# Performance work log

Hardware: AMD Instinct MI355X
Metric: run time of the kernel (lower is better)

Reference implementation:

```python
import jax, jax.numpy as jnp
import numpy as np

N_NODES = 100000


def setup_inputs() -> dict:
    key = jax.random.key(0)
    k1, k2, k3, k4, k5, k6 = jax.random.split(key, 6)
    N, E, DIN, DOUT = N_NODES, 1600000, 64, 64
    feature = jax.random.normal(k1, (N, DIN), dtype=jnp.float32)
    norm = jax.random.uniform(k2, (N, 1), dtype=jnp.float32)  # per-node 1/sqrt(deg)-style norm
    src = jax.random.randint(k3, (E,), 0, N, dtype=jnp.int32)
    dst = jax.random.randint(k4, (E,), 0, N, dtype=jnp.int32)
    W = jax.random.normal(k5, (DOUT, DIN), dtype=jnp.float32) / jnp.sqrt(jnp.float32(DIN))
    b = jax.random.normal(k6, (DOUT,), dtype=jnp.float32)
    return {"feature": feature, "norm": norm, "src": src, "dst": dst, "W": W, "b": b}


def reference(feature, norm, src, dst, W, b):
    # message: h_src * norm_src, gathered per edge -> [E, DIN]
    msg = (feature * norm)[src]
    # reduce: scatter-sum over destination nodes, then renormalize by dst norm
    accum = jax.ops.segment_sum(msg, dst, num_segments=N_NODES) * norm  # [N, DIN]
    # final Linear: accum @ W^T + b
    return accum @ W.T + b
```

## Files before the change

kernel.cpp:

```cpp
#include <hip/hip_runtime.h>
#include <hip/hip_bf16.h>

#define N_NODES 100000
#define D 64
#define BNODES 128
#define NBKT 782
#define SCAP 16
#define SCAP2 32
#define FIXU 256
#define CAP 48
#define SENT 0xFFFFFFFFu

__global__ __launch_bounds__(1024) void pre_scatter_kernel(
    const float* __restrict__ feature,
    const float* __restrict__ norm,
    const float* __restrict__ W,
    const int* __restrict__ src, const int* __restrict__ dst,
    __hip_bfloat16* __restrict__ Zb,
    unsigned int* __restrict__ f1,
    unsigned int* __restrict__ f2,
    unsigned char* __restrict__ cnt,
    int E)
{
    __shared__ float Wt[D * 65];
    __shared__ unsigned int stage[NBKT][17];
    __shared__ int scnt[NBKT];

    const int bid = blockIdx.x;
    const int tid = threadIdx.x;

    for (int i = tid; i < NBKT; i += blockDim.x) scnt[i] = 0;
    for (int i = tid; i < D * D; i += blockDim.x) {
        int o = i >> 6, k = i & 63;
        Wt[k * 65 + o] = W[o * D + k];
    }
    __syncthreads();

    const int lane = tid & 63;
    const int wid  = tid >> 6;

    float wreg[D];
    #pragma unroll
    for (int k = 0; k < D; ++k) wreg[k] = Wt[k * 65 + lane];

    const int wave   = bid * 16 + wid;
    const int nwaves = FIXU * 16;
    for (int node = wave; node < N_NODES; node += nwaves) {
        const int nu = __builtin_amdgcn_readfirstlane(node);
        const float* __restrict__ fp = feature + (size_t)nu * D;
        float r = 0.f;
        #pragma unroll
        for (int j = 0; j < D / 4; ++j) {
            float4 a4 = *(const float4*)&fp[j * 4];
            r = fmaf(a4.x, wreg[4 * j + 0], r);
            r = fmaf(a4.y, wreg[4 * j + 1], r);
            r = fmaf(a4.z, wreg[4 * j + 2], r);
            r = fmaf(a4.w, wreg[4 * j + 3], r);
        }
        Zb[(size_t)nu * D + lane] = __float2bfloat16(r * norm[nu]);
    }

    const size_t ubase = (size_t)bid * NBKT;
    const int nthreads = FIXU * 1024;
    for (int e = bid * 1024 + tid; e < E; e += nthreads) {
        int t = dst[e];
        int b = t >> 7;
        unsigned u = ((unsigned)src[e] << 7) | (unsigned)(t & 127);
        int slot = atomicAdd(&scnt[b], 1);
        if (slot < SCAP) {
            stage[b][slot] = u;
        } else if (slot < SCAP2) {
            f2[(ubase + (size_t)b) * 16 + (slot - SCAP)] = u;
        }
    }
    __syncthreads();

    for (int idx = tid; idx < NBKT * 4; idx += blockDim.x) {
        int bb = idx >> 2, j = idx & 3;
        int n_live = scnt[bb];
        if (n_live > SCAP) n_live = SCAP;
        int base = j * 4;
        unsigned v0 = (base + 0 < n_live) ? stage[bb][base + 0] : SENT;
        unsigned v1 = (base + 1 < n_live) ? stage[bb][base + 1] : SENT;
        unsigned v2 = (base + 2 < n_live) ? stage[bb][base + 2] : SENT;
        unsigned v3 = (base + 3 < n_live) ? stage[bb][base + 3] : SENT;
        *(uint4*)&f1[(ubase + (size_t)bb) * 16 + base] =
            make_uint4(v0, v1, v2, v3);
    }
    for (int bb = tid; bb < NBKT; bb += blockDim.x) {
        int n = scnt[bb];
        if (n > SCAP2) n = SCAP2;
        cnt[(size_t)bb * FIXU + bid] = (unsigned char)n;
    }
}

__device__ inline float2 bf2f(unsigned int z) {
    float2 r;
    r.x = __uint_as_float(z << 16);
    r.y = __uint_as_float(z & 0xffff0000u);
    return r;
}

__global__ __launch_bounds__(512) void csr_gather_kernel(
    const __hip_bfloat16* __restrict__ Zb,
    const float* __restrict__ norm,
    const unsigned int* __restrict__ f1,
    const unsigned int* __restrict__ f2,
    const unsigned char* __restrict__ cnt,
    const float* __restrict__ bias,
    float* __restrict__ out)
{
    __shared__ int slab[BNODES * CAP];
    __shared__ int lcnt[BNODES];

    const int b   = blockIdx.x;
    const int tid = threadIdx.x;

    for (int i = tid; i < BNODES; i += blockDim.x) lcnt[i] = 0;
    __syncthreads();

    const unsigned char* cn = cnt + (size_t)b * FIXU;

    for (int idx = tid; idx < FIXU * 4; idx += blockDim.x) {
        int bk = idx >> 2, j = idx & 3;
        int n = (int)cn[bk];
        if (n > SCAP) n = SCAP;
        int base = j * 4;
        if (base < n) {
            uint4 u4 = *(const uint4*)&f1[((size_t)bk * NBKT + (size_t)b) * 16 + base];
            int m = n - base; if (m > 4) m = 4;
            unsigned us[4] = {u4.x, u4.y, u4.z, u4.w};
            #pragma unroll
            for (int k = 0; k < 4; ++k) {
                if (k < m) {
                    unsigned u = us[k];
                    int local = (int)(u & 127);
                    int pos = atomicAdd(&lcnt[local], 1);
                    if (pos < CAP) slab[local * CAP + pos] = (int)(u >> 7);
                }
            }
        }
    }
    for (int bk = tid; bk < FIXU; bk += blockDim.x) {
        int n = (int)cn[bk];
        if (n > SCAP) {
            int m = n - SCAP;
            const unsigned int* sp = &f2[((size_t)bk * NBKT + (size_t)b) * 16];
            for (int t = 0; t < m; ++t) {
                unsigned u = sp[t];
                int local = (int)(u & 127);
                int pos = atomicAdd(&lcnt[local], 1);
                if (pos < CAP) slab[local * CAP + pos] = (int)(u >> 7);
            }
        }
    }
    __syncthreads();

    const int lane = tid & 63;
    const int wid  = tid >> 6;
    const int q    = lane >> 4;
    const int c    = lane & 15;

    const float4 bi = *(const float4*)&bias[4 * c];

    for (int nl = wid; nl < BNODES; nl += 8) {
        int node = (b << 7) + nl;
        if (node >= N_NODES) continue;

        int len = lcnt[nl];
        if (len > CAP) len = CAP;
        const int* sl = &slab[nl * CAP];

        float ax = 0.f, ay = 0.f, az = 0.f, aw = 0.f;
        int i = 0;
        for (; i + 16 <= len; i += 16) {
            int s0 = sl[i + 0  + q];
            int s1 = sl[i + 4  + q];
            int s2 = sl[i + 8  + q];
            int s3 = sl[i + 12 + q];
            uint2 z0 = *(const uint2*)&Zb[s0 * D + 4 * c];
            uint2 z1 = *(const uint2*)&Zb[s1 * D + 4 * c];
            uint2 z2 = *(const uint2*)&Zb[s2 * D + 4 * c];
            uint2 z3 = *(const uint2*)&Zb[s3 * D + 4 * c];
            float2 a0 = bf2f(z0.x), b0 = bf2f(z0.y);
            float2 a1 = bf2f(z1.x), b1 = bf2f(z1.y);
            float2 a2 = bf2f(z2.x), b2 = bf2f(z2.y);
            float2 a3 = bf2f(z3.x), b3 = bf2f(z3.y);
            ax += a0.x + a1.x + a2.x + a3.x;
            ay += a0.y + a1.y + a2.y + a3.y;
            az += b0.x + b1.x + b2.x + b3.x;
            aw += b0.y + b1.y + b2.y + b3.y;
        }
        for (; i < len; i += 4) {
            int idx = i + q;
            if (idx < len) {
                int s = sl[idx];
                uint2 z = *(const uint2*)&Zb[s * D + 4 * c];
                float2 a = bf2f(z.x), bb2 = bf2f(z.y);
                ax += a.x; ay += a.y; az += bb2.x; aw += bb2.y;
            }
        }

        ax += __shfl(ax, lane ^ 16, 64);
        ay += __shfl(ay, lane ^ 16, 64);
        az += __shfl(az, lane ^ 16, 64);
        aw += __shfl(aw, lane ^ 16, 64);
        ax += __shfl(ax, lane ^ 32, 64);
        ay += __shfl(ay, lane ^ 32, 64);
        az += __shfl(az, lane ^ 32, 64);
        aw += __shfl(aw, lane ^ 32, 64);

        if (q == 0) {
            float nv = norm[node];
            float4 o;
            o.x = fmaf(nv, ax, bi.x);
            o.y = fmaf(nv, ay, bi.y);
            o.z = fmaf(nv, az, bi.z);
            o.w = fmaf(nv, aw, bi.w);
            *(float4*)&out[node * D + 4 * c] = o;
        }
    }
}

extern "C" void kernel_launch(void* const* d_in, const int* in_sizes, int n_in,
                              void* d_out, int out_size, void* d_ws, size_t ws_size,
                              hipStream_t stream)
{
    const float* feature = (const float*)d_in[0];
    const float* norm    = (const float*)d_in[1];
    const int*   src     = (const int*)d_in[2];
    const int*   dst     = (const int*)d_in[3];
    const float* W       = (const float*)d_in[4];
    const float* b       = (const float*)d_in[5];
    float*       out     = (float*)d_out;

    const int E = in_sizes[2];

    char* p = (char*)d_ws;
    __hip_bfloat16* Zb = (__hip_bfloat16*)p;  p += (size_t)N_NODES * D * 2;
    unsigned int*   f1 = (unsigned int*)p;    p += (size_t)FIXU * NBKT * 16 * 4;
    unsigned int*   f2 = (unsigned int*)p;    p += (size_t)FIXU * NBKT * 16 * 4;
    unsigned char*  cnt = (unsigned char*)p;

    pre_scatter_kernel<<<FIXU, 1024, 0, stream>>>(
        feature, norm, W, src, dst, Zb, f1, f2, cnt, E);

    csr_gather_kernel<<<NBKT, 512, 0, stream>>>(Zb, norm, f1, f2, cnt, b, out);
}
```

Measured before the change: 156.7 us.

## Fuse scatter and gather into one cooperative kernel with grid sync

Merges the pre-scatter and CSR-gather kernels into a single cooperative kernel of 256 blocks of 1024 threads, separated by a grid-wide barrier. The gather phase splits each block into two 512-thread halves, each with its own shared-memory slab, and loops two rounds to cover the 782 buckets. This removes one kernel launch and the gap between launches. The cost is cooperative launch overhead, a grid barrier, and lower parallelism in the gather phase, since 512 half-blocks now cover 782 buckets instead of 782 separate blocks.

```diff
diff --git a/kernel.cpp b/kernel.cpp
--- a/kernel.cpp
+++ b/kernel.cpp
@@ -1,5 +1,8 @@
 #include <hip/hip_runtime.h>
 #include <hip/hip_bf16.h>
+#include <hip/hip_cooperative_groups.h>
+
+namespace cg = cooperative_groups;
 
 #define N_NODES 100000
 #define D 64
@@ -11,7 +14,22 @@
 #define CAP 48
 #define SENT 0xFFFFFFFFu
 
-__global__ __launch_bounds__(1024) void pre_scatter_kernel(
+#define WT_BYTES    (D * 65 * 4)
+#define STAGE_OFF   WT_BYTES
+#define STAGE_BYTES (NBKT * 17 * 4)
+#define SCNT_OFF    (STAGE_OFF + STAGE_BYTES)
+#define POOL_BYTES  (SCNT_OFF + NBKT * 4)
+#define SLAB_BYTES  (BNODES * CAP * 4)
+#define LCNT_OFF    (2 * SLAB_BYTES)
+
+__device__ inline float2 bf2f(unsigned int z) {
+    float2 r;
+    r.x = __uint_as_float(z << 16);
+    r.y = __uint_as_float(z & 0xffff0000u);
+    return r;
+}
+
+__global__ __launch_bounds__(1024) void mega_kernel(
     const float* __restrict__ feature,
     const float* __restrict__ norm,
     const float* __restrict__ W,
@@ -20,204 +38,209 @@
     unsigned int* __restrict__ f1,
     unsigned int* __restrict__ f2,
     unsigned char* __restrict__ cnt,
+    const float* __restrict__ bias,
+    float* __restrict__ out,
     int E)
 {
-    __shared__ float Wt[D * 65];
-    __shared__ unsigned int stage[NBKT][17];
-    __shared__ int scnt[NBKT];
+    __shared__ __align__(16) char pool[POOL_BYTES];
 
     const int bid = blockIdx.x;
     const int tid = threadIdx.x;
 
-    for (int i = tid; i < NBKT; i += blockDim.x) scnt[i] = 0;
-    for (int i = tid; i < D * D; i += blockDim.x) {
-        int o = i >> 6, k = i & 63;
-        Wt[k * 65 + o] = W[o * D + k];
+    {
+        float* Wt = (float*)pool;
+        unsigned int (*stage)[17] = (unsigned int (*)[17])(pool + STAGE_OFF);
+        int* scnt = (int*)(pool + SCNT_OFF);
+
+        for (int i = tid; i < NBKT; i += blockDim.x) scnt[i] = 0;
+        for (int i = tid; i < D * D; i += blockDim.x) {
+            int o = i >> 6, k = i & 63;
+            Wt[k * 65 + o] = W[o * D + k];
+        }
+        __syncthreads();
+
+        const int lane = tid & 63;
+        const int wid  = tid >> 6;
+
+        float wreg[D];
+        #pragma unroll
+        for (int k = 0; k < D; ++k) wreg[k] = Wt[k * 65 + lane];
+
+        const int wave   = bid * 16 + wid;
+        const int nwaves = FIXU * 16;
+        for (int node = wave; node < N_NODES; node += nwaves) {
+            const int nu = __builtin_amdgcn_readfirstlane(node);
+            const float* __restrict__ fp = feature + (size_t)nu * D;
+            float r = 0.f;
+            #pragma unroll
+            for (int j = 0; j < D / 4; ++j) {
+                float4 a4 = *(const float4*)&fp[j * 4];
+                r = fmaf(a4.x, wreg[4 * j + 0], r);
+                r = fmaf(a4.y, wreg[4 * j + 1], r);
+                r = fmaf(a4.z, wreg[4 * j + 2], r);
+                r = fmaf(a4.w, wreg[4 * j + 3], r);
+            }
+            Zb[(size_t)nu * D + lane] = __float2bfloat16(r * norm[nu]);
+        }
+
+        const size_t ubase = (size_t)bid * NBKT;
+        const int nthreads = FIXU * 1024;
+        for (int e = bid * 1024 + tid; e < E; e += nthreads) {
+            int t = dst[e];
+            int b = t >> 7;
+            unsigned u = ((unsigned)src[e] << 7) | (unsigned)(t & 127);
+            int slot = atomicAdd(&scnt[b], 1);
+            if (slot < SCAP) {
+                stage[b][slot] = u;
+            } else if (slot < SCAP2) {
+                f2[(ubase + (size_t)b) * 16 + (slot - SCAP)] = u;
+            }
+        }
+        __syncthreads();
+
+        for (int idx = tid; idx < NBKT * 4; idx += blockDim.x) {
+            int bb = idx >> 2, j = idx & 3;
+            int n_live = scnt[bb];
+            if (n_live > SCAP) n_live = SCAP;
+            int base = j * 4;
+            unsigned v0 = (base + 0 < n_live) ? stage[bb][base + 0] : SENT;
+            unsigned v1 = (base + 1 < n_live) ? stage[bb][base + 1] : SENT;
+            unsigned v2 = (base + 2 < n_live) ? stage[bb][base + 2] : SENT;
+            unsigned v3 = (base + 3 < n_live) ? stage[bb][base + 3] : SENT;
+            *(uint4*)&f1[(ubase + (size_t)bb) * 16 + base] =
+                make_uint4(v0, v1, v2, v3);
+        }
+        for (int bb = tid; bb < NBKT; bb += blockDim.x) {
+            int n = scnt[bb];
+            if (n > SCAP2) n = SCAP2;
+            cnt[(size_t)bb * FIXU + bid] = (unsigned char)n;
+        }
     }
-    __syncthreads();
-
-    const int lane = tid & 63;
-    const int wid  = tid >> 6;
-
-    float wreg[D];
-    #pragma unroll
-    for (int k = 0; k < D; ++k) wreg[k] = Wt[k * 65 + lane];
-
-    const int wave   = bid * 16 + wid;
-    const int nwaves = FIXU * 16;
-    for (int node = wave; node < N_NODES; node += nwaves) {
-        const int nu = __builtin_amdgcn_readfirstlane(node);
-        const float* __restrict__ fp = feature + (size_t)nu * D;
-        float r = 0.f;
-        #pragma unroll
-        for (int j = 0; j < D / 4; ++j) {
-            float4 a4 = *(const float4*)&fp[j * 4];
-            r = fmaf(a4.x, wreg[4 * j + 0], r);
-            r = fmaf(a4.y, wreg[4 * j + 1], r);
-            r = fmaf(a4.z, wreg[4 * j + 2], r);
-            r = fmaf(a4.w, wreg[4 * j + 3], r);
-        }
-        Zb[(size_t)nu * D + lane] = __float2bfloat16(r * norm[nu]);
-    }
-
-    const size_t ubase = (size_t)bid * NBKT;
-    const int nthreads = FIXU * 1024;
-    for (int e = bid * 1024 + tid; e < E; e += nthreads) {
-        int t = dst[e];
-        int b = t >> 7;
-        unsigned u = ((unsigned)src[e] << 7) | (unsigned)(t & 127);
-        int slot = atomicAdd(&scnt[b], 1);
-        if (slot < SCAP) {
-            stage[b][slot] = u;
-        } else if (slot < SCAP2) {
-            f2[(ubase + (size_t)b) * 16 + (slot - SCAP)] = u;
-        }
-    }
-    __syncthreads();
-
-    for (int idx = tid; idx < NBKT * 4; idx += blockDim.x) {
-        int bb = idx >> 2, j = idx & 3;
-        int n_live = scnt[bb];
-        if (n_live > SCAP) n_live = SCAP;
-        int base = j * 4;
-        unsigned v0 = (base + 0 < n_live) ? stage[bb][base + 0] : SENT;
-        unsigned v1 = (base + 1 < n_live) ? stage[bb][base + 1] : SENT;
-        unsigned v2 = (base + 2 < n_live) ? stage[bb][base + 2] : SENT;
-        unsigned v3 = (base + 3 < n_live) ? stage[bb][base + 3] : SENT;
-        *(uint4*)&f1[(ubase + (size_t)bb) * 16 + base] =
-            make_uint4(v0, v1, v2, v3);
-    }
-    for (int bb = tid; bb < NBKT; bb += blockDim.x) {
-        int n = scnt[bb];
-        if (n > SCAP2) n = SCAP2;
-        cnt[(size_t)bb * FIXU + bid] = (unsigned char)n;
-    }
-}
-
-__device__ inline float2 bf2f(unsigned int z) {
-    float2 r;
-    r.x = __uint_as_float(z << 16);
-    r.y = __uint_as_float(z & 0xffff0000u);
-    return r;
-}
-
-__global__ __launch_bounds__(512) void csr_gather_kernel(
-    const __hip_bfloat16* __restrict__ Zb,
-    const float* __restrict__ norm,
-    const unsigned int* __restrict__ f1,
-    const unsigned int* __restrict__ f2,
-    const unsigned char* __restrict__ cnt,
-    const float* __restrict__ bias,
-    float* __restrict__ out)
-{
-    __shared__ int slab[BNODES * CAP];
-    __shared__ int lcnt[BNODES];
-
-    const int b   = blockIdx.x;
-    const int tid = threadIdx.x;
-
-    for (int i = tid; i < BNODES; i += blockDim.x) lcnt[i] = 0;
-    __syncthreads();
-
-    const unsigned char* cn = cnt + (size_t)b * FIXU;
-
-    for (int idx = tid; idx < FIXU * 4; idx += blockDim.x) {
-        int bk = idx >> 2, j = idx & 3;
-        int n = (int)cn[bk];
-        if (n > SCAP) n = SCAP;
-        int base = j * 4;
-        if (base < n) {
-            uint4 u4 = *(const uint4*)&f1[((size_t)bk * NBKT + (size_t)b) * 16 + base];
-            int m = n - base; if (m > 4) m = 4;
-            unsigned us[4] = {u4.x, u4.y, u4.z, u4.w};
-            #pragma unroll
-            for (int k = 0; k < 4; ++k) {
-                if (k < m) {
-                    unsigned u = us[k];
-                    int local = (int)(u & 127);
-                    int pos = atomicAdd(&lcnt[local], 1);
-                    if (pos < CAP) slab[local * CAP + pos] = (int)(u >> 7);
+
+    cg::this_grid().sync();
+
+    {
+        const int half = tid >> 9;
+        const int t5   = tid & 511;
+        const int h    = (bid << 1) | half;
+        int* slab = (int*)(pool + half * SLAB_BYTES);
+        int* lcnt = (int*)(pool + LCNT_OFF + half * (BNODES * 4));
+
+        const int lane = t5 & 63;
+        const int wid  = t5 >> 6;
+        const int q    = lane >> 4;
+        const int c    = lane & 15;
+        const float4 bi = *(const float4*)&bias[4 * c];
+
+        for (int round = 0; round < 2; ++round) {
+            const int bkt = h + round * 512;
+            const bool active = bkt < NBKT;
+
+            __syncthreads();
+            if (active) {
+                for (int i = t5; i < BNODES; i += 512) lcnt[i] = 0;
+            }
+            __syncthreads();
+
+            if (active) {
+                const unsigned char* cn = cnt + (size_t)bkt * FIXU;
+                for (int idx = t5; idx < FIXU * 4; idx += 512) {
+                    int bk = idx >> 2, j = idx & 3;
+                    int n = (int)cn[bk];
+                    if (n > SCAP) n = SCAP;
+                    int base = j * 4;
+                    if (base < n) {
+                        uint4 u4 = *(const uint4*)
+                            &f1[((size_t)bk * NBKT + (size_t)bkt) * 16 + base];
+                        int m = n - base; if (m > 4) m = 4;
+                        unsigned us[4] = {u4.x, u4.y, u4.z, u4.w};
+                        #pragma unroll
+                        for (int k = 0; k < 4; ++k) {
+                            if (k < m) {
+                                unsigned u = us[k];
+                                int local = (int)(u & 127);
+                                int pos = atomicAdd(&lcnt[local], 1);
+                                if (pos < CAP) slab[local * CAP + pos] = (int)(u >> 7);
+                            }
+                        }
+                    }
                 }
-            }
-        }
-    }
-    for (int bk = tid; bk < FIXU; bk += blockDim.x) {
-        int n = (int)cn[bk];
-        if (n > SCAP) {
-            int m = n - SCAP;
-            const unsigned int* sp = &f2[((size_t)bk * NBKT + (size_t)b) * 16];
-            for (int t = 0; t < m; ++t) {
-                unsigned u = sp[t];
-                int local = (int)(u & 127);
-                int pos = atomicAdd(&lcnt[local], 1);
-                if (pos < CAP) slab[local * CAP + pos] = (int)(u >> 7);
-            }
-        }
-    }
-    __syncthreads();
-
-    const int lane = tid & 63;
-    const int wid  = tid >> 6;
-    const int q    = lane >> 4;
-    const int c    = lane & 15;
-
-    const float4 bi = *(const float4*)&bias[4 * c];
-
-    for (int nl = wid; nl < BNODES; nl += 8) {
-        int node = (b << 7) + nl;
-        if (node >= N_NODES) continue;
-
-        int len = lcnt[nl];
-        if (len > CAP) len = CAP;
-        const int* sl = &slab[nl * CAP];
-
-        float ax = 0.f, ay = 0.f, az = 0.f, aw = 0.f;
-        int i = 0;
-        for (; i + 16 <= len; i += 16) {
-            int s0 = sl[i + 0  + q];
-            int s1 = sl[i + 4  + q];
-            int s2 = sl[i + 8  + q];
-            int s3 = sl[i + 12 + q];
-            uint2 z0 = *(const uint2*)&Zb[s0 * D + 4 * c];
-            uint2 z1 = *(const uint2*)&Zb[s1 * D + 4 * c];
-            uint2 z2 = *(const uint2*)&Zb[s2 * D + 4 * c];
-            uint2 z3 = *(const uint2*)&Zb[s3 * D + 4 * c];
-            float2 a0 = bf2f(z0.x), b0 = bf2f(z0.y);
-            float2 a1 = bf2f(z1.x), b1 = bf2f(z1.y);
-            float2 a2 = bf2f(z2.x), b2 = bf2f(z2.y);
-            float2 a3 = bf2f(z3.x), b3 = bf2f(z3.y);
-            ax += a0.x + a1.x + a2.x + a3.x;
-            ay += a0.y + a1.y + a2.y + a3.y;
-            az += b0.x + b1.x + b2.x + b3.x;
-            aw += b0.y + b1.y + b2.y + b3.y;
-        }
-        for (; i < len; i += 4) {
-            int idx = i + q;
-            if (idx < len) {
-                int s = sl[idx];
-                uint2 z = *(const uint2*)&Zb[s * D + 4 * c];
-                float2 a = bf2f(z.x), bb2 = bf2f(z.y);
-                ax += a.x; ay += a.y; az += bb2.x; aw += bb2.y;
-            }
-        }
-
-        ax += __shfl(ax, lane ^ 16, 64);
-        ay += __shfl(ay, lane ^ 16, 64);
-        az += __shfl(az, lane ^ 16, 64);
-        aw += __shfl(aw, lane ^ 16, 64);
-        ax += __shfl(ax, lane ^ 32, 64);
-        ay += __shfl(ay, lane ^ 32, 64);
-        az += __shfl(az, lane ^ 32, 64);
-        aw += __shfl(aw, lane ^ 32, 64);
-
-        if (q == 0) {
-            float nv = norm[node];
-            float4 o;
-            o.x = fmaf(nv, ax, bi.x);
-            o.y = fmaf(nv, ay, bi.y);
-            o.z = fmaf(nv, az, bi.z);
-            o.w = fmaf(nv, aw, bi.w);
-            *(float4*)&out[node * D + 4 * c] = o;
+                for (int bk = t5; bk < FIXU; bk += 512) {
+                    int n = (int)cn[bk];
+                    if (n > SCAP) {
+                        int m = n - SCAP;
+                        const unsigned int* sp =
+                            &f2[((size_t)bk * NBKT + (size_t)bkt) * 16];
+                        for (int t = 0; t < m; ++t) {
+                            unsigned u = sp[t];
+                            int local = (int)(u & 127);
+                            int pos = atomicAdd(&lcnt[local], 1);
+                            if (pos < CAP) slab[local * CAP + pos] = (int)(u >> 7);
+                        }
+                    }
+                }
+            }
+            __syncthreads();
+
+            if (active) {
+                for (int nl = wid; nl < BNODES; nl += 8) {
+                    int node = (bkt << 7) + nl;
+                    if (node >= N_NODES) continue;
+
+                    int len = lcnt[nl];
+                    if (len > CAP) len = CAP;
+                    const int* sl = &slab[nl * CAP];
+
+                    float ax = 0.f, ay = 0.f, az = 0.f, aw = 0.f;
+                    int i = 0;
+                    for (; i + 16 <= len; i += 16) {
+                        int s0 = sl[i + 0  + q];
+                        int s1 = sl[i + 4  + q];
+                        int s2 = sl[i + 8  + q];
+                        int s3 = sl[i + 12 + q];
+                        uint2 z0 = *(const uint2*)&Zb[s0 * D + 4 * c];
+                        uint2 z1 = *(const uint2*)&Zb[s1 * D + 4 * c];
+                        uint2 z2 = *(const uint2*)&Zb[s2 * D + 4 * c];
+                        uint2 z3 = *(const uint2*)&Zb[s3 * D + 4 * c];
+                        float2 a0 = bf2f(z0.x), b0 = bf2f(z0.y);
+                        float2 a1 = bf2f(z1.x), b1 = bf2f(z1.y);
+                        float2 a2 = bf2f(z2.x), b2 = bf2f(z2.y);
+                        float2 a3 = bf2f(z3.x), b3 = bf2f(z3.y);
+                        ax += a0.x + a1.x + a2.x + a3.x;
+                        ay += a0.y + a1.y + a2.y + a3.y;
+                        az += b0.x + b1.x + b2.x + b3.x;
+                        aw += b0.y + b1.y + b2.y + b3.y;
+                    }
+                    for (; i < len; i += 4) {
+                        int idx = i + q;
+                        if (idx < len) {
+                            int s = sl[idx];
+                            uint2 z = *(const uint2*)&Zb[s * D + 4 * c];
+                            float2 a = bf2f(z.x), bb2 = bf2f(z.y);
+                            ax += a.x; ay += a.y; az += bb2.x; aw += bb2.y;
+                        }
+                    }
+
+                    ax += __shfl(ax, lane ^ 16, 64);
+                    ay += __shfl(ay, lane ^ 16, 64);
+                    az += __shfl(az, lane ^ 16, 64);
+                    aw += __shfl(aw, lane ^ 16, 64);
+                    ax += __shfl(ax, lane ^ 32, 64);
+                    ay += __shfl(ay, lane ^ 32, 64);
+                    az += __shfl(az, lane ^ 32, 64);
+                    aw += __shfl(aw, lane ^ 32, 64);
+
+                    if (q == 0) {
+                        float nv = norm[node];
+                        float4 o;
+                        o.x = fmaf(nv, ax, bi.x);
+                        o.y = fmaf(nv, ay, bi.y);
+                        o.z = fmaf(nv, az, bi.z);
+                        o.w = fmaf(nv, aw, bi.w);
+                        *(float4*)&out[node * D + 4 * c] = o;
+                    }
+                }
+            }
         }
     }
 }
@@ -231,10 +254,10 @@
     const int*   src     = (const int*)d_in[2];
     const int*   dst     = (const int*)d_in[3];
     const float* W       = (const float*)d_in[4];
-    const float* b       = (const float*)d_in[5];
+    const float* bias    = (const float*)d_in[5];
     float*       out     = (float*)d_out;
 
-    const int E = in_sizes[2];
+    int E = in_sizes[2];
 
     char* p = (char*)d_ws;
     __hip_bfloat16* Zb = (__hip_bfloat16*)p;  p += (size_t)N_NODES * D * 2;
@@ -242,8 +265,10 @@
     unsigned int*   f2 = (unsigned int*)p;    p += (size_t)FIXU * NBKT * 16 * 4;
     unsigned char*  cnt = (unsigned char*)p;
 
-    pre_scatter_kernel<<<FIXU, 1024, 0, stream>>>(
-        feature, norm, W, src, dst, Zb, f1, f2, cnt, E);
-
-    csr_gather_kernel<<<NBKT, 512, 0, stream>>>(Zb, norm, f1, f2, cnt, b, out);
+    void* args[] = {(void*)&feature, (void*)&norm, (void*)&W,
+                    (void*)&src, (void*)&dst, (void*)&Zb,
+                    (void*)&f1, (void*)&f2, (void*)&cnt,
+                    (void*)&bias, (void*)&out, (void*)&E};
+    hipLaunchCooperativeKernel((const void*)mega_kernel,
+                               dim3(FIXU), dim3(1024), args, 0, stream);
 }
```

New measurement: 231.7 us. +47.9%, slower.
